# Kernel optimization log

Hardware: AMD Instinct MI355X
Metric: run time of the kernel (lower is better)

## Reference

```python
import jax, jax.numpy as jnp
import numpy as np

NUM_EMBEDDINGS = 1000
EMBEDDING_DIM = 64
COMMITMENT_COST = 10.0


def setup_inputs() -> dict:
    key = jax.random.key(0)
    k1, k2 = jax.random.split(key)
    x = jax.random.normal(k1, (16, EMBEDDING_DIM, 2048), dtype=jnp.float32)  # [B, D, L]
    emb_w = jax.random.normal(k2, (NUM_EMBEDDINGS, EMBEDDING_DIM), dtype=jnp.float32)
    return {"x": x, "emb_w": emb_w}


def reference(x, emb_w):
    # [B, D, L] -> [B, L, D]
    inputs = jnp.transpose(x, (0, 2, 1))
    B, L, D = inputs.shape
    K = emb_w.shape[0]
    flat = inputs.reshape(-1, D)  # [N, D]

    # squared L2 distances to every codebook vector: [N, K]
    distances = (
        jnp.sum(flat * flat, axis=1, keepdims=True)
        + jnp.sum(emb_w * emb_w, axis=1)
        - 2.0 * jnp.matmul(flat, emb_w.T)
    )
    idx = jnp.argmin(distances, axis=1)  # [N]

    # direct gather instead of one-hot matmul (same math)
    quantized = emb_w[idx].reshape(B, L, D)

    e_latent_loss = jnp.mean((jax.lax.stop_gradient(quantized) - inputs) ** 2)
    q_latent_loss = jnp.mean((quantized - jax.lax.stop_gradient(inputs)) ** 2)
    loss = q_latent_loss + COMMITMENT_COST * e_latent_loss

    # straight-through estimator
    quantized_st = inputs + jax.lax.stop_gradient(quantized - inputs)

    counts = jnp.zeros((K,), dtype=jnp.int32).at[idx].add(1)
    embedding_usage = jnp.sum(counts > 0)

    out = jnp.transpose(quantized_st, (0, 2, 1))  # back to [B, D, L]
    return out, loss, embedding_usage, idx[:, None]
```

## Files before the change

### kernel.cpp

```cpp
#include <hip/hip_runtime.h>

using v4f = float __attribute__((ext_vector_type(4)));

constexpr int NTOK = 32768;
constexpr int DIMS = 64;
constexpr int KCODES = 1000;
constexpr int TPB = 128;
constexpr int CHUNK = 128;
constexpr int CPS = 4;
constexpr float BIG = 3.4e38f;

__global__ void vq_prep(const float* __restrict__ emb, float* __restrict__ norms,
                        float* __restrict__ loss_accum, int* __restrict__ usage)
{
    int gid = blockIdx.x * 256 + threadIdx.x;
    if (gid == 0) *loss_accum = 0.f;
    if (gid < KCODES) {
        usage[gid] = 0;
        const float* e = emb + gid * DIMS;
        float s = 0.f;
        #pragma unroll
        for (int d4 = 0; d4 < 16; ++d4) {
            v4f q = *reinterpret_cast<const v4f*>(e + d4 * 4);
            s = fmaf(q[0], q[0], s);
            s = fmaf(q[1], q[1], s);
            s = fmaf(q[2], q[2], s);
            s = fmaf(q[3], q[3], s);
        }
        norms[gid] = s;
    }
}

__global__ __launch_bounds__(256, 2) void vq_argmin(
    const float* __restrict__ x, const float* __restrict__ emb,
    const float* __restrict__ norms,
    float* __restrict__ pval, int* __restrict__ pidx)
{
    __shared__ float xs[DIMS][TPB];
    __shared__ float es[CHUNK][68];
    __shared__ float ns[CHUNK];

    const int tid   = threadIdx.x;
    const int tblk  = blockIdx.x >> 1;
    const int split = blockIdx.x & 1;
    const int tok0  = tblk * TPB;
    const int b     = tok0 >> 11;
    const int l0    = tok0 & 2047;
    const float* xbase = x + ((size_t)b << 17) + l0;

    #pragma unroll
    for (int it = 0; it < 8; ++it) {
        int f  = it * 256 + tid;
        int d  = f >> 5;
        int t4 = (f & 31) << 2;
        *reinterpret_cast<v4f*>(&xs[d][t4]) =
            *reinterpret_cast<const v4f*>(xbase + d * 2048 + t4);
    }

    const int ty = tid >> 4;
    const int tx = tid & 15;

    float minv[8];
    int   mini[8];
    #pragma unroll
    for (int i = 0; i < 8; ++i) { minv[i] = BIG; mini[i] = 0; }

    for (int cc = 0; cc < CPS; ++cc) {
        const int cbase = (split * CPS + cc) * CHUNK;
        __syncthreads();
        #pragma unroll
        for (int it = 0; it < 8; ++it) {
            int f  = it * 256 + tid;
            int c  = f >> 4;
            int d4 = (f & 15) << 2;
            int gc = cbase + c;
            v4f v = {0.f, 0.f, 0.f, 0.f};
            if (gc < KCODES) v = *reinterpret_cast<const v4f*>(emb + gc * DIMS + d4);
            *reinterpret_cast<v4f*>(&es[c][d4]) = v;
        }
        if (tid < CHUNK) {
            int gc = cbase + tid;
            ns[tid] = (gc < KCODES) ? norms[gc] : 3.0e38f;
        }
        __syncthreads();

        float acc[8][8];
        #pragma unroll
        for (int i = 0; i < 8; ++i)
            #pragma unroll
            for (int j = 0; j < 8; ++j) acc[i][j] = 0.f;

        #pragma unroll 4
        for (int d4 = 0; d4 < 16; ++d4) {
            const int d0 = d4 * 4;
            v4f xa[4], xb[4];
            #pragma unroll
            for (int dd = 0; dd < 4; ++dd) {
                xa[dd] = *reinterpret_cast<const v4f*>(&xs[d0 + dd][ty * 8]);
                xb[dd] = *reinterpret_cast<const v4f*>(&xs[d0 + dd][ty * 8 + 4]);
            }
            #pragma unroll
            for (int j = 0; j < 8; ++j) {
                v4f ev = *reinterpret_cast<const v4f*>(&es[tx + 16 * j][d0]);
                #pragma unroll
                for (int dd = 0; dd < 4; ++dd) {
                    const float e = ev[dd];
                    acc[0][j] = fmaf(xa[dd][0], e, acc[0][j]);
                    acc[1][j] = fmaf(xa[dd][1], e, acc[1][j]);
                    acc[2][j] = fmaf(xa[dd][2], e, acc[2][j]);
                    acc[3][j] = fmaf(xa[dd][3], e, acc[3][j]);
                    acc[4][j] = fmaf(xb[dd][0], e, acc[4][j]);
                    acc[5][j] = fmaf(xb[dd][1], e, acc[5][j]);
                    acc[6][j] = fmaf(xb[dd][2], e, acc[6][j]);
                    acc[7][j] = fmaf(xb[dd][3], e, acc[7][j]);
                }
            }
        }

        #pragma unroll
        for (int j = 0; j < 8; ++j) {
            const int c = tx + 16 * j;
            const float nv = ns[c];
            const int gi = cbase + c;
            #pragma unroll
            for (int i = 0; i < 8; ++i) {
                float dist = fmaf(-2.f, acc[i][j], nv);
                if (dist < minv[i]) { minv[i] = dist; mini[i] = gi; }
            }
        }
    }

    #pragma unroll
    for (int i = 0; i < 8; ++i) {
        float v = minv[i];
        int  ix = mini[i];
        #pragma unroll
        for (int off = 8; off >= 1; off >>= 1) {
            float vo = __shfl_xor(v, off);
            int   io = __shfl_xor(ix, off);
            if (vo < v || (vo == v && io < ix)) { v = vo; ix = io; }
        }
        if (tx == 0) {
            int token = tok0 + ty * 8 + i;
            pval[split * NTOK + token] = v;
            pidx[split * NTOK + token] = ix;
        }
    }
}

__global__ __launch_bounds__(256) void vq_output(
    const float* __restrict__ x, const float* __restrict__ emb,
    const float* __restrict__ pval, const int* __restrict__ pidx,
    float* __restrict__ out, float* __restrict__ idx_f,
    float* __restrict__ loss_accum, int* __restrict__ usage)
{
    const int tid   = threadIdx.x;
    const int token = blockIdx.x * 256 + tid;
    const float v0 = pval[token];
    const float v1 = pval[NTOK + token];
    const int   i0 = pidx[token];
    const int   i1 = pidx[NTOK + token];
    const int   ix = (v1 < v0) ? i1 : i0;

    idx_f[token] = (float)ix;
    usage[ix] = 1;

    const int b = token >> 11, l = token & 2047;
    const float* xb = x   + ((size_t)b << 17) + l;
    float*       ob = out + ((size_t)b << 17) + l;
    const float* e  = emb + ix * DIMS;

    float lsum = 0.f;
    #pragma unroll
    for (int d4 = 0; d4 < 16; ++d4) {
        v4f q = *reinterpret_cast<const v4f*>(e + d4 * 4);
        #pragma unroll
        for (int dd = 0; dd < 4; ++dd) {
            const int d = d4 * 4 + dd;
            float xv = xb[(size_t)d * 2048];
            float diff = q[dd] - xv;
            lsum += diff * diff;
            ob[(size_t)d * 2048] = xv + diff;
        }
    }

    #pragma unroll
    for (int off = 32; off >= 1; off >>= 1) lsum += __shfl_xor(lsum, off);
    __shared__ float bsum[4];
    if ((tid & 63) == 0) bsum[tid >> 6] = lsum;
    __syncthreads();
    if (tid == 0) atomicAdd(loss_accum, bsum[0] + bsum[1] + bsum[2] + bsum[3]);
}

__global__ void vq_finalize(const float* __restrict__ loss_accum, const int* __restrict__ usage,
                            float* __restrict__ o_loss, float* __restrict__ o_usage)
{
    __shared__ int wsum[16];
    int tid = threadIdx.x;
    int c = (tid < KCODES && usage[tid]) ? 1 : 0;
    #pragma unroll
    for (int off = 32; off >= 1; off >>= 1) c += __shfl_xor(c, off);
    if ((tid & 63) == 0) wsum[tid >> 6] = c;
    __syncthreads();
    if (tid == 0) {
        int total = 0;
        #pragma unroll
        for (int i = 0; i < 16; ++i) total += wsum[i];
        float s = *loss_accum;
        float m = s / 2097152.0f;
        o_loss[0]  = m + 10.0f * m;
        o_usage[0] = (float)total;
    }
}

extern "C" void kernel_launch(void* const* d_in, const int* in_sizes, int n_in,
                              void* d_out, int out_size, void* d_ws, size_t ws_size,
                              hipStream_t stream)
{
    const float* x   = (const float*)d_in[0];
    const float* emb = (const float*)d_in[1];

    float* o       = (float*)d_out;
    float* out     = o;
    float* o_loss  = o + 2097152;
    float* o_usage = o + 2097153;
    float* o_idx   = o + 2097154;

    char*  ws         = (char*)d_ws;
    float* loss_accum = (float*)(ws);
    int*   usage      = (int*)(ws + 64);
    float* norms      = (float*)(ws + 4096);
    float* pval       = (float*)(ws + 8192);
    int*   pidx       = (int*)(ws + 8192 + 2 * NTOK * sizeof(float));

    vq_prep<<<4, 256, 0, stream>>>(emb, norms, loss_accum, usage);
    vq_argmin<<<512, 256, 0, stream>>>(x, emb, norms, pval, pidx);
    vq_output<<<NTOK / 256, 256, 0, stream>>>(x, emb, pval, pidx, out, o_idx, loss_accum, usage);
    vq_finalize<<<1, 1024, 0, stream>>>(loss_accum, usage, o_loss, o_usage);
}
```

Before: 136.3 us.

## Split codebook four ways, read x from global, swizzle LDS, fuse finalize

The argmin kernel now splits the 1000 codes across 4 block groups instead of 2, so it launches 1024 blocks. It drops the shared-memory x tile and reads x straight from global memory inside the inner loop. The codebook tile in LDS uses an XOR swizzle instead of padding, and occupancy is raised to 4 blocks per CU. The finalize kernel is folded into the output kernel via a last-block counter, which removes one launch. Reading x from global in the hot loop risks more memory traffic and latency, and each token is now recomputed against four partial minima.

```diff
diff --git a/kernel.cpp b/kernel.cpp
--- a/kernel.cpp
+++ b/kernel.cpp
@@ -7,14 +7,16 @@
 constexpr int KCODES = 1000;
 constexpr int TPB = 128;
 constexpr int CHUNK = 128;
-constexpr int CPS = 4;
+constexpr int NSPLIT = 4;
+constexpr int NCHUNK = 2;
 constexpr float BIG = 3.4e38f;
 
 __global__ void vq_prep(const float* __restrict__ emb, float* __restrict__ norms,
-                        float* __restrict__ loss_accum, int* __restrict__ usage)
+                        float* __restrict__ loss_accum, int* __restrict__ usage,
+                        int* __restrict__ counter)
 {
     int gid = blockIdx.x * 256 + threadIdx.x;
-    if (gid == 0) *loss_accum = 0.f;
+    if (gid == 0) { *loss_accum = 0.f; *counter = 0; }
     if (gid < KCODES) {
         usage[gid] = 0;
         const float* e = emb + gid * DIMS;
@@ -31,56 +33,47 @@
     }
 }
 
-__global__ __launch_bounds__(256, 2) void vq_argmin(
+__global__ __launch_bounds__(256, 4) void vq_argmin(
     const float* __restrict__ x, const float* __restrict__ emb,
     const float* __restrict__ norms,
     float* __restrict__ pval, int* __restrict__ pidx)
 {
-    __shared__ float xs[DIMS][TPB];
-    __shared__ float es[CHUNK][68];
+    __shared__ float es[CHUNK * DIMS];
     __shared__ float ns[CHUNK];
 
     const int tid   = threadIdx.x;
-    const int tblk  = blockIdx.x >> 1;
-    const int split = blockIdx.x & 1;
+    const int split = blockIdx.x >> 8;
+    const int tblk  = blockIdx.x & 255;
     const int tok0  = tblk * TPB;
     const int b     = tok0 >> 11;
     const int l0    = tok0 & 2047;
-    const float* xbase = x + ((size_t)b << 17) + l0;
-
-    #pragma unroll
-    for (int it = 0; it < 8; ++it) {
-        int f  = it * 256 + tid;
-        int d  = f >> 5;
-        int t4 = (f & 31) << 2;
-        *reinterpret_cast<v4f*>(&xs[d][t4]) =
-            *reinterpret_cast<const v4f*>(xbase + d * 2048 + t4);
-    }
+    const float* xg = x + ((size_t)b << 17) + l0;
 
     const int ty = tid >> 4;
     const int tx = tid & 15;
+    const float* xrow = xg + ty * 8;
 
     float minv[8];
     int   mini[8];
     #pragma unroll
     for (int i = 0; i < 8; ++i) { minv[i] = BIG; mini[i] = 0; }
 
-    for (int cc = 0; cc < CPS; ++cc) {
-        const int cbase = (split * CPS + cc) * CHUNK;
+    for (int cc = 0; cc < NCHUNK; ++cc) {
+        const int cbase = split * (NCHUNK * CHUNK) + cc * CHUNK;
         __syncthreads();
         #pragma unroll
         for (int it = 0; it < 8; ++it) {
             int f  = it * 256 + tid;
             int c  = f >> 4;
-            int d4 = (f & 15) << 2;
-            int gc = cbase + c;
+            int d4 = f & 15;
+            int g  = cbase + c;
             v4f v = {0.f, 0.f, 0.f, 0.f};
-            if (gc < KCODES) v = *reinterpret_cast<const v4f*>(emb + gc * DIMS + d4);
-            *reinterpret_cast<v4f*>(&es[c][d4]) = v;
+            if (g < KCODES) v = *reinterpret_cast<const v4f*>(emb + g * DIMS + d4 * 4);
+            *reinterpret_cast<v4f*>(es + c * 64 + 4 * (d4 ^ (c & 7))) = v;
         }
         if (tid < CHUNK) {
-            int gc = cbase + tid;
-            ns[tid] = (gc < KCODES) ? norms[gc] : 3.0e38f;
+            int g = cbase + tid;
+            ns[tid] = (g < KCODES) ? norms[g] : BIG;
         }
         __syncthreads();
 
@@ -96,12 +89,13 @@
             v4f xa[4], xb[4];
             #pragma unroll
             for (int dd = 0; dd < 4; ++dd) {
-                xa[dd] = *reinterpret_cast<const v4f*>(&xs[d0 + dd][ty * 8]);
-                xb[dd] = *reinterpret_cast<const v4f*>(&xs[d0 + dd][ty * 8 + 4]);
+                xa[dd] = *reinterpret_cast<const v4f*>(xrow + (size_t)(d0 + dd) * 2048);
+                xb[dd] = *reinterpret_cast<const v4f*>(xrow + (size_t)(d0 + dd) * 2048 + 4);
             }
             #pragma unroll
             for (int j = 0; j < 8; ++j) {
-                v4f ev = *reinterpret_cast<const v4f*>(&es[tx + 16 * j][d0]);
+                const int c = tx + 16 * j;
+                v4f ev = *reinterpret_cast<const v4f*>(es + c * 64 + 4 * (d4 ^ (c & 7)));
                 #pragma unroll
                 for (int dd = 0; dd < 4; ++dd) {
                     const float e = ev[dd];
@@ -119,7 +113,7 @@
 
         #pragma unroll
         for (int j = 0; j < 8; ++j) {
-            const int c = tx + 16 * j;
+            const int c  = tx + 16 * j;
             const float nv = ns[c];
             const int gi = cbase + c;
             #pragma unroll
@@ -148,68 +142,70 @@
     }
 }
 
-__global__ __launch_bounds__(256) void vq_output(
+__global__ __launch_bounds__(128) void vq_output(
     const float* __restrict__ x, const float* __restrict__ emb,
     const float* __restrict__ pval, const int* __restrict__ pidx,
     float* __restrict__ out, float* __restrict__ idx_f,
-    float* __restrict__ loss_accum, int* __restrict__ usage)
+    float* __restrict__ loss_accum, int* __restrict__ usage,
+    int* __restrict__ counter, float* __restrict__ o_scalars)
 {
     const int tid   = threadIdx.x;
-    const int token = blockIdx.x * 256 + tid;
-    const float v0 = pval[token];
-    const float v1 = pval[NTOK + token];
-    const int   i0 = pidx[token];
-    const int   i1 = pidx[NTOK + token];
-    const int   ix = (v1 < v0) ? i1 : i0;
-
-    idx_f[token] = (float)ix;
-    usage[ix] = 1;
+    const int token = blockIdx.x * 128 + tid;
+
+    float bv = pval[token];
+    int   bi = pidx[token];
+    #pragma unroll
+    for (int s = 1; s < NSPLIT; ++s) {
+        float v = pval[s * NTOK + token];
+        int   i2 = pidx[s * NTOK + token];
+        if (v < bv) { bv = v; bi = i2; }
+    }
+    idx_f[token] = (float)bi;
+    atomicOr(&usage[bi], 1);
 
     const int b = token >> 11, l = token & 2047;
     const float* xb = x   + ((size_t)b << 17) + l;
     float*       ob = out + ((size_t)b << 17) + l;
-    const float* e  = emb + ix * DIMS;
+    const float* e  = emb + bi * DIMS;
 
     float lsum = 0.f;
-    #pragma unroll
-    for (int d4 = 0; d4 < 16; ++d4) {
-        v4f q = *reinterpret_cast<const v4f*>(e + d4 * 4);
-        #pragma unroll
-        for (int dd = 0; dd < 4; ++dd) {
-            const int d = d4 * 4 + dd;
-            float xv = xb[(size_t)d * 2048];
-            float diff = q[dd] - xv;
-            lsum += diff * diff;
-            ob[(size_t)d * 2048] = xv + diff;
-        }
+    #pragma unroll 8
+    for (int d = 0; d < DIMS; ++d) {
+        float xv   = xb[(size_t)d * 2048];
+        float diff = e[d] - xv;
+        lsum = fmaf(diff, diff, lsum);
+        ob[(size_t)d * 2048] = xv + diff;
     }
 
     #pragma unroll
     for (int off = 32; off >= 1; off >>= 1) lsum += __shfl_xor(lsum, off);
-    __shared__ float bsum[4];
+    __shared__ float bsum[2];
     if ((tid & 63) == 0) bsum[tid >> 6] = lsum;
     __syncthreads();
-    if (tid == 0) atomicAdd(loss_accum, bsum[0] + bsum[1] + bsum[2] + bsum[3]);
-}
-
-__global__ void vq_finalize(const float* __restrict__ loss_accum, const int* __restrict__ usage,
-                            float* __restrict__ o_loss, float* __restrict__ o_usage)
-{
-    __shared__ int wsum[16];
-    int tid = threadIdx.x;
-    int c = (tid < KCODES && usage[tid]) ? 1 : 0;
-    #pragma unroll
-    for (int off = 32; off >= 1; off >>= 1) c += __shfl_xor(c, off);
-    if ((tid & 63) == 0) wsum[tid >> 6] = c;
+    if (tid == 0) atomicAdd(loss_accum, bsum[0] + bsum[1]);
+
+    __threadfence();
+    __shared__ int last;
+    if (tid == 0) last = (atomicAdd(counter, 1) == (int)gridDim.x - 1);
     __syncthreads();
-    if (tid == 0) {
-        int total = 0;
-        #pragma unroll
-        for (int i = 0; i < 16; ++i) total += wsum[i];
-        float s = *loss_accum;
-        float m = s / 2097152.0f;
-        o_loss[0]  = m + 10.0f * m;
-        o_usage[0] = (float)total;
+    if (last) {
+        int c = 0;
+        #pragma unroll
+        for (int k = 0; k < 8; ++k) {
+            int u = tid * 8 + k;
+            if (u < KCODES) c += atomicAdd(&usage[u], 0);
+        }
+        #pragma unroll
+        for (int off = 32; off >= 1; off >>= 1) c += __shfl_xor(c, off);
+        __shared__ int csum[2];
+        if ((tid & 63) == 0) csum[tid >> 6] = c;
+        __syncthreads();
+        if (tid == 0) {
+            float s = atomicAdd(loss_accum, 0.0f);
+            float m = s / 2097152.0f;
+            o_scalars[0] = 11.0f * m;
+            o_scalars[1] = (float)(csum[0] + csum[1]);
+        }
     }
 }
 
@@ -222,19 +218,19 @@
 
     float* o       = (float*)d_out;
     float* out     = o;
-    float* o_loss  = o + 2097152;
-    float* o_usage = o + 2097153;
+    float* o_scal  = o + 2097152;
     float* o_idx   = o + 2097154;
 
     char*  ws         = (char*)d_ws;
     float* loss_accum = (float*)(ws);
+    int*   counter    = (int*)(ws + 8);
     int*   usage      = (int*)(ws + 64);
-    float* norms      = (float*)(ws + 4096);
+    float* norms      = (float*)(ws + 4160);
     float* pval       = (float*)(ws + 8192);
-    int*   pidx       = (int*)(ws + 8192 + 2 * NTOK * sizeof(float));
-
-    vq_prep<<<4, 256, 0, stream>>>(emb, norms, loss_accum, usage);
-    vq_argmin<<<512, 256, 0, stream>>>(x, emb, norms, pval, pidx);
-    vq_output<<<NTOK / 256, 256, 0, stream>>>(x, emb, pval, pidx, out, o_idx, loss_accum, usage);
-    vq_finalize<<<1, 1024, 0, stream>>>(loss_accum, usage, o_loss, o_usage);
-}
+    int*   pidx       = (int*)(ws + 8192 + NSPLIT * NTOK * sizeof(float));
+
+    vq_prep<<<4, 256, 0, stream>>>(emb, norms, loss_accum, usage, counter);
+    vq_argmin<<<NSPLIT * 256, 256, 0, stream>>>(x, emb, norms, pval, pidx);
+    vq_output<<<NTOK / 128, 128, 0, stream>>>(x, emb, pval, pidx, out, o_idx,
+                                              loss_accum, usage, counter, o_scal);
+}
```

Result: slower. 292.7 us (+114.8%).
